# Performance work log

Measured on AMD Instinct MI355X. Metric: run time of the kernel, lower is better.

The kernel has to match this reference:

```python
import jax, jax.numpy as jnp
from jax import lax
import numpy as np

B, N, M, C, K = 2, 16384, 4096, 16, 32
RADIUS = 0.1
EPS = 1e-8


def setup_inputs() -> dict:
    key = jax.random.key(0)
    ks = jax.random.split(key, 9)
    return {
        "xyz": jax.random.uniform(ks[0], (B, N, 3), jnp.float32),
        "new_xyz": jax.random.uniform(ks[1], (B, M, 3), jnp.float32),
        "features": jax.random.normal(ks[2], (B, C, N), jnp.float32),
        "w0": jax.random.normal(ks[3], (32, C), jnp.float32) * 0.1,
        "b0": jax.random.normal(ks[4], (32,), jnp.float32) * 0.1,
        "w1": jax.random.normal(ks[5], (64, 32), jnp.float32) * 0.1,
        "b1": jax.random.normal(ks[6], (64,), jnp.float32) * 0.1,
        "wxyz": jax.random.normal(ks[7], (32, 3), jnp.float32) * 0.1,
        "bxyz": jax.random.normal(ks[8], (32,), jnp.float32) * 0.1,
    }


def ball_query(xyz, new_xyz, radius, nsample):
    """Return (idx [B,M,K] int32, idn multiplicity [B,M,K] int32, has_any [B,M] bool).
    Matches pointnet2 ball_query: first `nsample` in-radius indices (ascending),
    empty slots padded with the first found index; idn counts how many times an
    index is duplicated in a row (0 everywhere for rows with no neighbor)."""
    d2 = jnp.sum((new_xyz[:, :, None, :] - xyz[:, None, :, :]) ** 2, axis=-1)  # B,M,N
    n = xyz.shape[1]
    score = jnp.where(d2 < radius * radius,
                      jnp.arange(n, dtype=jnp.int32), jnp.int32(n))
    idx = -lax.top_k(-score, nsample)[0]          # B,M,K smallest indices, asc
    valid = idx < n
    idx = jnp.where(valid, idx, idx[..., :1])      # pad with first found index
    has_any = valid[..., 0]
    idx = jnp.where(idx >= n, 0, idx)              # safe gather for empty rows
    cnt = jnp.sum(idx[..., :, None] == idx[..., None, :], axis=-1).astype(jnp.int32)
    idn = jnp.where(has_any[..., None], cnt, 0)
    return idx, idn, has_any


def reference(xyz, new_xyz, features, w0, b0, w1, b1, wxyz, bxyz):
    idx, idn, has_any = ball_query(xyz, new_xyz, RADIUS, K)
    b_idx = jnp.arange(xyz.shape[0])[:, None, None]
    # QueryAndGroup: relative coords + gathered features
    rel = xyz[b_idx, idx] - new_xyz[:, :, None, :]            # B,M,K,3
    rel = jnp.transpose(rel, (0, 3, 1, 2))                    # B,3,M,K
    gfeat = jnp.transpose(features, (0, 2, 1))[b_idx, idx]    # B,M,K,C
    gfeat = jnp.transpose(gfeat, (0, 3, 1, 2))                # B,C,M,K

    # distance-reciprocal weights, duplicate-corrected by idn, row-normalized
    dist = jnp.linalg.norm(rel, axis=1, keepdims=True)        # B,1,M,K
    dist_recip = 1.0 / (dist + EPS)
    _idn = jnp.where(has_any[:, None, :, None], idn[:, None, :, :], 1).astype(dist.dtype)
    dist_recip = dist_recip / _idn
    weights = dist_recip / jnp.sum(dist_recip, axis=3, keepdims=True)
    idn_mask = has_any[:, None, :, None].astype(dist.dtype)
    weights = weights * idn_mask                              # zero empty rows

    # SharedMLP on features: 1x1 conv == per-point matmul, ReLU
    h = jax.nn.relu(jnp.einsum('bcmk,oc->bomk', gfeat, w0) + b0[None, :, None, None])
    h = jax.nn.relu(jnp.einsum('bcmk,oc->bomk', h, w1) + b1[None, :, None, None])
    feat_sum = jnp.sum(weights * h, axis=3)                   # B,64,M weighted sum-pool

    # xyz branch: SharedMLP [3,32] + max-pool over neighbors
    hx = jax.nn.relu(jnp.einsum('bcmk,oc->bomk', rel, wxyz) + bxyz[None, :, None, None])
    feat_max = jnp.max(hx, axis=3)                            # B,32,M

    return new_xyz, jnp.concatenate([feat_max, feat_sum], axis=1)  # (B,M,3),(B,96,M)
```

## Files before the change

kernel.cpp:

```cpp
#include <hip/hip_runtime.h>
#include <math.h>
#include <limits.h>

#define BB 2
#define NN 16384
#define MM 4096
#define CCH 16
#define KK 32
#define R2 0.01f
#define EPSV 1e-8f
#define GD 10
#define CPB (GD*GD*GD)
#define CAP 56
#define NCELL (BB*CPB)
#define WSA_OFF 8192
#define WSB_OFF 10240
#define BUCKET_OFF 16384
#define FEATT_OFF (2*1024*1024)
#define WS_GRID (BUCKET_OFF + (size_t)NCELL*CAP*16)
#define WS_FT   (FEATT_OFF + (size_t)BB*NN*CCH*2)
#define NDW 512
#define TBL 768
#define HST 40

typedef __attribute__((ext_vector_type(8))) short short8;
typedef __attribute__((ext_vector_type(4))) float v4f;

__device__ __forceinline__ short f2bf(float f) {
    unsigned u = __float_as_uint(f);
    unsigned r = u + 0x7FFFu + ((u >> 16) & 1u);
    return (short)(r >> 16);
}
__device__ __forceinline__ unsigned pk2(float a, float b) {
    return (unsigned)(unsigned short)f2bf(a) | ((unsigned)(unsigned short)f2bf(b) << 16);
}

__device__ __forceinline__ int cell_of(float x, float y, float z) {
    int cx = min(GD-1, max(0, (int)(x * 10.0f)));
    int cy = min(GD-1, max(0, (int)(y * 10.0f)));
    int cz = min(GD-1, max(0, (int)(z * 10.0f)));
    return (cx*GD + cy)*GD + cz;
}

__global__ void k_scatter(const float* __restrict__ xyz, const float* __restrict__ feat,
                          const float* __restrict__ w0, const float* __restrict__ w1,
                          int* __restrict__ cnt, int* __restrict__ ovf,
                          float4* __restrict__ buckets,
                          short8* __restrict__ wsA, short8* __restrict__ wsB,
                          uint4* __restrict__ ftb, int use_ft) {
    if (blockIdx.x == 0) {
        int t = threadIdx.x;
        if (t < 128) {
            int fi = t >> 6, l = t & 63, l15 = l & 15, qd = (l >> 4) & 3;
            short8 a = {0,0,0,0,0,0,0,0};
            if (qd < 2)
                #pragma unroll
                for (int j = 0; j < 8; ++j)
                    a[j] = f2bf(w0[(fi*16 + l15)*CCH + qd*8 + j]);
            wsA[fi*64 + l] = a;
        }
        if (t < 64) {
            int l15 = t & 15, qd = t >> 4;
            #pragma unroll
            for (int u = 0; u < 4; ++u) {
                const float* wr = w1 + ((u << 4) + l15)*32 + (qd << 3);
                short8 bb;
                #pragma unroll
                for (int j = 0; j < 8; ++j) bb[j] = f2bf(wr[j]);
                wsB[t*4 + u] = bb;
            }
        }
    }
    int i = blockIdx.x*256 + threadIdx.x;
    if (i >= BB*NN) return;
    const float* p = xyz + (size_t)i*3;
    int b = i >> 14;
    int n = i & (NN-1);
    float x = p[0], y = p[1], z = p[2];
    int cell = b*CPB + cell_of(x, y, z);
    int slot = atomicAdd(&cnt[cell], 1);
    if (slot < CAP)
        buckets[(size_t)cell*CAP + slot] = make_float4(x, y, z, __int_as_float(n));
    else
        *ovf = 1;
    if (use_ft) {
        const float* fb = feat + (size_t)b*CCH*NN + n;
        unsigned d[8];
        #pragma unroll
        for (int c2 = 0; c2 < 8; ++c2)
            d[c2] = pk2(fb[(2*c2)*NN], fb[(2*c2+1)*NN]);
        ftb[(size_t)i*2 + 0] = make_uint4(d[0], d[1], d[2], d[3]);
        ftb[(size_t)i*2 + 1] = make_uint4(d[4], d[5], d[6], d[7]);
    }
}

__global__ __launch_bounds__(256, 4) void grouper_fused(
    const float* __restrict__ xyz, const float* __restrict__ new_xyz,
    const float* __restrict__ feat,
    const float* __restrict__ w0, const float* __restrict__ b0,
    const float* __restrict__ w1, const float* __restrict__ b1,
    const float* __restrict__ wxyz, const float* __restrict__ bxyz,
    const int* __restrict__ cnt, const int* __restrict__ ovf,
    const float4* __restrict__ buckets,
    const short8* __restrict__ wsA, const short8* __restrict__ wsB,
    const short8* __restrict__ ftb,
    int use_grid, int use_ft,
    float* __restrict__ out)
{
    const int lane = threadIdx.x & 63;
    const int wid  = threadIdx.x >> 6;
    const int q    = (blockIdx.x << 2) + wid;
    const int b    = q >> 12;
    const int m    = q & (MM - 1);

    __shared__ int s_idx[4][KK];
    __shared__ float4 s_rel[4][KK];
    __shared__ __align__(16) unsigned s_bm[4][NDW];
    __shared__ __align__(16) int s_tbl[4][TBL];

    const float* xb = xyz + (size_t)b * NN * 3;
    const float qx = new_xyz[((size_t)b*MM + m)*3 + 0];
    const float qy = new_xyz[((size_t)b*MM + m)*3 + 1];
    const float qz = new_xyz[((size_t)b*MM + m)*3 + 2];
    const unsigned long long below = (1ull << lane) - 1ull;

    int nfound = 0, idx0 = 0;
    bool need_full = (use_grid == 0) || (use_grid && ovf[0] != 0);

    if (!need_full) {
        uint4 z4 = make_uint4(0u, 0u, 0u, 0u);
        *(uint4*)&s_bm[wid][lane*8]     = z4;
        *(uint4*)&s_bm[wid][lane*8 + 4] = z4;

        int x0 = max(0, (int)floorf((qx - 0.1f)*10.0f - 1e-3f));
        int x1 = min(GD-1, (int)floorf((qx + 0.1f)*10.0f + 1e-3f));
        int y0 = max(0, (int)floorf((qy - 0.1f)*10.0f - 1e-3f));
        int y1 = min(GD-1, (int)floorf((qy + 0.1f)*10.0f + 1e-3f));
        int z0 = max(0, (int)floorf((qz - 0.1f)*10.0f - 1e-3f));
        int z1 = min(GD-1, (int)floorf((qz + 0.1f)*10.0f + 1e-3f));

        const int nzc = z1 - z0 + 1, nyc = y1 - y0 + 1, nxc = x1 - x0 + 1;
        const int nyz = nyc * nzc;
        const int ncells = nxc * nyz;
        int myCnt = 0, myBase = 0;
        if (lane < ncells) {
            const float rnyz = 1.0f / (float)nyz;
            const float rnz  = 1.0f / (float)nzc;
            int cxr = (int)((float)lane * rnyz + 1e-4f);
            int rem = lane - cxr * nyz;
            int cyr = (int)((float)rem * rnz + 1e-4f);
            int czr = rem - cyr * nzc;
            int cx = x0 + cxr, cy = y0 + cyr, cz = z0 + czr;
            float xlo = cx*0.1f, ylo = cy*0.1f, zlo = cz*0.1f;
            float ddx = fmaxf(fmaxf(xlo - qx, qx - (xlo + 0.1f)), 0.0f);
            float ddy = fmaxf(fmaxf(ylo - qy, qy - (ylo + 0.1f)), 0.0f);
            float ddz = fmaxf(fmaxf(zlo - qz, qz - (zlo + 0.1f)), 0.0f);
            if (ddx*ddx + ddy*ddy + ddz*ddz < R2) {
                int cell = b*CPB + (cx*GD + cy)*GD + cz;
                myCnt = min(cnt[cell], CAP);
                myBase = cell*CAP;
            }
        }

        int incl = myCnt;
        #pragma unroll
        for (int d = 1; d < 64; d <<= 1) {
            int t = __shfl_up(incl, d);
            if (lane >= d) incl += t;
        }
        const int total = __shfl(incl, 63);
        const int wbase = incl - myCnt;

        if (total > TBL) {
            need_full = true;
        } else {
            int* tbl = &s_tbl[wid][0];
            for (int t = 0; t < myCnt; ++t) tbl[wbase + t] = myBase + t;
            __builtin_amdgcn_wave_barrier();

            const int iters = (total + 63) >> 6;
            int j = lane;
            bool v0 = (j < total);
            int sl0 = v0 ? tbl[j] : 0;
            float4 p0 = make_float4(0.f, 0.f, 0.f, 0.f);
            if (v0) p0 = buckets[sl0];
            for (int it = 0; it < iters; ++it) {
                int jn = j + 64;
                bool v1 = (jn < total);
                int sl1 = v1 ? tbl[jn] : 0;
                float4 pn = make_float4(0.f, 0.f, 0.f, 0.f);
                if (v1) pn = buckets[sl1];
                if (v0) {
                    float dx = p0.x - qx, dy = p0.y - qy, dz = p0.z - qz;
                    if (dx*dx + dy*dy + dz*dz < R2) {
                        int id = __float_as_int(p0.w);
                        atomicOr(&s_bm[wid][id >> 5], 1u << (id & 31));
                    }
                }
                j = jn; v0 = v1; sl0 = sl1; p0 = pn;
            }

            __builtin_amdgcn_wave_barrier();

            uint4 d0 = *(uint4*)&s_bm[wid][lane*8];
            uint4 d1 = *(uint4*)&s_bm[wid][lane*8 + 4];
            unsigned dw[8] = {d0.x, d0.y, d0.z, d0.w, d1.x, d1.y, d1.z, d1.w};
            int pc = 0;
            #pragma unroll
            for (int jj = 0; jj < 8; ++jj) pc += __popc(dw[jj]);
            int pre = pc;
            #pragma unroll
            for (int d = 1; d < 64; d <<= 1) {
                int t = __shfl_up(pre, d);
                if (lane >= d) pre += t;
            }
            int tt = __shfl(pre, 63);
            int rank = pre - pc;
            nfound = min(tt, KK);

            if (rank < KK) {
                #pragma unroll
                for (int jj = 0; jj < 8; ++jj) {
                    unsigned bits = dw[jj];
                    while (bits && rank < KK) {
                        int bpos = __builtin_ctz(bits);
                        s_idx[wid][rank] = ((lane*8 + jj) << 5) + bpos;
                        bits &= bits - 1;
                        ++rank;
                    }
                }
            }

            __builtin_amdgcn_wave_barrier();
            idx0 = (nfound > 0) ? s_idx[wid][0] : 0;
            __builtin_amdgcn_wave_barrier();
            if (lane >= nfound && lane < KK) s_idx[wid][lane] = idx0;
            __builtin_amdgcn_wave_barrier();
        }
    }

    if (need_full) {
        int cntf = 0;
        for (int basep = 0; basep < NN; basep += 256) {
            float d2a[4];
            #pragma unroll
            for (int j = 0; j < 4; ++j) {
                int i = basep + (j << 6) + lane;
                float px = xb[i*3+0], py = xb[i*3+1], pz = xb[i*3+2];
                float dx = px - qx, dy = py - qy, dz = pz - qz;
                d2a[j] = dx*dx + dy*dy + dz*dz;
            }
            #pragma unroll
            for (int j = 0; j < 4; ++j) {
                bool hit = d2a[j] < R2;
                unsigned long long msk = __ballot(hit);
                if (hit) {
                    int pos = cntf + __popcll(msk & below);
                    if (pos < KK) s_idx[wid][pos] = basep + (j << 6) + lane;
                }
                cntf += __popcll(msk);
            }
            if (cntf >= KK) break;
        }
        nfound = cntf < KK ? cntf : KK;
        __builtin_amdgcn_wave_barrier();
        if (lane < KK) {
            int v = 0;
            if (nfound > 0) v = (lane < nfound) ? s_idx[wid][lane] : s_idx[wid][0];
            s_idx[wid][lane] = v;
        }
        __builtin_amdgcn_wave_barrier();
        idx0 = s_idx[wid][0];
    }

    {
        const int k = lane & 31;
        const int h = lane >> 5;
        const int ik = s_idx[wid][k];
        float px = xb[ik*3+0], py = xb[ik*3+1], pz = xb[ik*3+2];
        float rx = px - qx, ry = py - qy, rz = pz - qz;
        float dist = sqrtf(rx*rx + ry*ry + rz*rz);
        float recip = 1.0f / (dist + EPSV);
        float mult = (float)(1 + KK - nfound);
        float w = recip / ((ik == idx0) ? mult : 1.0f);
        float S = w;
        #pragma unroll
        for (int d = 1; d < 32; d <<= 1) S += __shfl_xor(S, d);
        float wk = (nfound > 0) ? (w / S) : 0.0f;
        if (h == 0) s_rel[wid][k] = make_float4(rx, ry, rz, wk);
    }
    __builtin_amdgcn_wave_barrier();

    const int l15 = lane & 15;
    const int quad = lane >> 4;

    short8 A1, A1b, Bf[4];
    if (use_grid) {
        A1  = wsA[lane];
        A1b = wsA[64 + lane];
        #pragma unroll
        for (int u = 0; u < 4; ++u) Bf[u] = wsB[lane*4 + u];
    } else {
        short8 z = {0,0,0,0,0,0,0,0};
        A1 = z; A1b = z;
        if (quad < 2) {
            #pragma unroll
            for (int j = 0; j < 8; ++j) {
                A1[j]  = f2bf(w0[l15*CCH + quad*8 + j]);
                A1b[j] = f2bf(w0[(16 + l15)*CCH + quad*8 + j]);
            }
        }
        #pragma unroll
        for (int u = 0; u < 4; ++u) {
            const float* wr = w1 + ((u << 4) + l15)*32 + (quad << 3);
            #pragma unroll
            for (int j = 0; j < 8; ++j) Bf[u][j] = f2bf(wr[j]);
        }
    }

    short8 G0 = {0,0,0,0,0,0,0,0}, G1 = {0,0,0,0,0,0,0,0};
    if (quad < 2) {
        int ika = s_idx[wid][l15];
        int ikb = s_idx[wid][16 + l15];
        if (use_ft) {
            G0 = ftb[(size_t)(b*NN + ika)*2 + quad];
            G1 = ftb[(size_t)(b*NN + ikb)*2 + quad];
        } else {
            const float* fb = feat + (size_t)b * CCH * NN;
            int cb0 = quad << 3;
            #pragma unroll
            for (int j = 0; j < 8; ++j) {
                G0[j] = f2bf(fb[(cb0 + j)*NN + ika]);
                G1[j] = f2bf(fb[(cb0 + j)*NN + ikb]);
            }
        }
    }

    v4f C0, C1;
    #pragma unroll
    for (int r = 0; r < 4; ++r) {
        C0[r] = b0[(quad << 2) + r];
        C1[r] = b0[16 + (quad << 2) + r];
    }

    v4f H00 = __builtin_amdgcn_mfma_f32_16x16x32_bf16(A1,  G0, C0, 0, 0, 0);
    v4f H01 = __builtin_amdgcn_mfma_f32_16x16x32_bf16(A1b, G0, C1, 0, 0, 0);
    v4f H10 = __builtin_amdgcn_mfma_f32_16x16x32_bf16(A1,  G1, C0, 0, 0, 0);
    v4f H11 = __builtin_amdgcn_mfma_f32_16x16x32_bf16(A1b, G1, C1, 0, 0, 0);

    __builtin_amdgcn_wave_barrier();
    short* hb = (short*)&s_tbl[wid][0];
    {
        uint2 w;
        w.x = pk2(fmaxf(H00[0],0.f), fmaxf(H00[1],0.f));
        w.y = pk2(fmaxf(H00[2],0.f), fmaxf(H00[3],0.f));
        *(uint2*)&hb[l15*HST + (quad << 2)] = w;
        w.x = pk2(fmaxf(H01[0],0.f), fmaxf(H01[1],0.f));
        w.y = pk2(fmaxf(H01[2],0.f), fmaxf(H01[3],0.f));
        *(uint2*)&hb[l15*HST + 16 + (quad << 2)] = w;
        w.x = pk2(fmaxf(H10[0],0.f), fmaxf(H10[1],0.f));
        w.y = pk2(fmaxf(H10[2],0.f), fmaxf(H10[3],0.f));
        *(uint2*)&hb[(16 + l15)*HST + (quad << 2)] = w;
        w.x = pk2(fmaxf(H11[0],0.f), fmaxf(H11[1],0.f));
        w.y = pk2(fmaxf(H11[2],0.f), fmaxf(H11[3],0.f));
        *(uint2*)&hb[(16 + l15)*HST + 16 + (quad << 2)] = w;
    }
    __builtin_amdgcn_wave_barrier();

    short8 A2_0 = *(short8*)&hb[l15*HST + (quad << 3)];
    short8 A2_1 = *(short8*)&hb[(16 + l15)*HST + (quad << 3)];

    float wkv[2][4];
    #pragma unroll
    for (int t = 0; t < 2; ++t)
        #pragma unroll
        for (int r = 0; r < 4; ++r)
            wkv[t][r] = s_rel[wid][16*t + (quad << 2) + r].w;

    float* out2 = out + (size_t)BB*MM*3 + (size_t)b*96*MM;

    float Su[4];
    #pragma unroll
    for (int u = 0; u < 4; ++u) {
        float b1u = b1[(u << 4) + l15];
        v4f Cb = {b1u, b1u, b1u, b1u};
        v4f D0 = __builtin_amdgcn_mfma_f32_16x16x32_bf16(A2_0, Bf[u], Cb, 0, 0, 0);
        v4f D1 = __builtin_amdgcn_mfma_f32_16x16x32_bf16(A2_1, Bf[u], Cb, 0, 0, 0);
        float s = 0.f;
        #pragma unroll
        for (int r = 0; r < 4; ++r)
            s += wkv[0][r]*fmaxf(D0[r], 0.f) + wkv[1][r]*fmaxf(D1[r], 0.f);
        s += __shfl_xor(s, 16);
        s += __shfl_xor(s, 32);
        Su[u] = s;
    }
    float sout = (quad == 0) ? Su[0] : (quad == 1) ? Su[1] : (quad == 2) ? Su[2] : Su[3];
    out2[(32 + lane)*MM + m] = sout;

    {
        const int c = lane & 31;
        const int h = lane >> 5;
        const float wx0 = wxyz[c*3+0], wx1 = wxyz[c*3+1], wx2 = wxyz[c*3+2];
        const float bc = bxyz[c];
        float v = 0.0f;
        #pragma unroll
        for (int kk = 0; kk < 16; ++kk) {
            float4 hr = s_rel[wid][(h << 4) + kk];
            float t = bc + wx0*hr.x + wx1*hr.y + wx2*hr.z;
            v = fmaxf(v, fmaxf(t, 0.0f));
        }
        v = fmaxf(v, __shfl_xor(v, 32));
        if (h == 0) out2[c*MM + m] = v;
    }

    if (lane == 0) {
        float* o0 = out + ((size_t)b*MM + m)*3;
        o0[0] = qx; o0[1] = qy; o0[2] = qz;
    }
}

extern "C" void kernel_launch(void* const* d_in, const int* in_sizes, int n_in,
                              void* d_out, int out_size, void* d_ws, size_t ws_size,
                              hipStream_t stream) {
    const float* xyz     = (const float*)d_in[0];
    const float* new_xyz = (const float*)d_in[1];
    const float* feat    = (const float*)d_in[2];
    const float* w0      = (const float*)d_in[3];
    const float* b0      = (const float*)d_in[4];
    const float* w1      = (const float*)d_in[5];
    const float* b1      = (const float*)d_in[6];
    const float* wxyz    = (const float*)d_in[7];
    const float* bxyz    = (const float*)d_in[8];
    float* out = (float*)d_out;

    int* ovf = (int*)d_ws;
    int* cnt = (int*)((char*)d_ws + 64);
    short8* wsA = (short8*)((char*)d_ws + WSA_OFF);
    short8* wsB = (short8*)((char*)d_ws + WSB_OFF);
    float4* buckets = (float4*)((char*)d_ws + BUCKET_OFF);
    uint4* ftb4 = (uint4*)((char*)d_ws + FEATT_OFF);
    const short8* ftb = (const short8*)((char*)d_ws + FEATT_OFF);
    const int use_grid = (d_ws != nullptr && ws_size >= WS_GRID) ? 1 : 0;
    const int use_ft   = (d_ws != nullptr && ws_size >= WS_FT) ? 1 : 0;

    if (use_grid) {
        hipMemsetAsync(d_ws, 0, BUCKET_OFF, stream);
        hipLaunchKernelGGL(k_scatter, dim3((BB*NN+255)/256), dim3(256), 0, stream,
                           xyz, feat, w0, w1, cnt, ovf, buckets, wsA, wsB, ftb4, use_ft);
    }
    hipLaunchKernelGGL(grouper_fused, dim3((BB*MM)/4), dim3(256), 0, stream,
                       xyz, new_xyz, feat, w0, b0, w1, b1, wxyz, bxyz,
                       cnt, ovf, buckets, wsA, wsB, ftb, use_grid, use_ft, out);
}
```

Baseline: 96.46 us.

## Share bitmap and table LDS scratch, raise occupancy, deepen bucket prefetch

Merges the per-wave bitmap and cell-slot table into one shared scratch region, shrinking the table cap from 768 to 512 entries, and raises launch bounds from 4 to 8 blocks per CU. The aim is more resident waves to hide the latency of the global bucket gathers. The candidate loop now prefetches two iterations ahead instead of one, and the memset is cut to only the counter/flag region. Queries whose candidate count exceeds 512 now fall back to the slow full scan more often, and the tighter register budget may cause spills.

```diff
diff --git a/kernel.cpp b/kernel.cpp
--- a/kernel.cpp
+++ b/kernel.cpp
@@ -20,7 +20,7 @@
 #define WS_GRID (BUCKET_OFF + (size_t)NCELL*CAP*16)
 #define WS_FT   (FEATT_OFF + (size_t)BB*NN*CCH*2)
 #define NDW 512
-#define TBL 768
+#define TBL 512
 #define HST 40
 
 typedef __attribute__((ext_vector_type(8))) short short8;
@@ -94,7 +94,7 @@
     }
 }
 
-__global__ __launch_bounds__(256, 4) void grouper_fused(
+__global__ __launch_bounds__(256, 8) void grouper_fused(
     const float* __restrict__ xyz, const float* __restrict__ new_xyz,
     const float* __restrict__ feat,
     const float* __restrict__ w0, const float* __restrict__ b0,
@@ -115,8 +115,10 @@
 
     __shared__ int s_idx[4][KK];
     __shared__ float4 s_rel[4][KK];
-    __shared__ __align__(16) unsigned s_bm[4][NDW];
-    __shared__ __align__(16) int s_tbl[4][TBL];
+    __shared__ __align__(16) unsigned s_scr[4][1024];
+
+    unsigned* bm = &s_scr[wid][0];
+    int* tbl = (int*)&s_scr[wid][NDW];
 
     const float* xb = xyz + (size_t)b * NN * 3;
     const float qx = new_xyz[((size_t)b*MM + m)*3 + 0];
@@ -129,8 +131,8 @@
 
     if (!need_full) {
         uint4 z4 = make_uint4(0u, 0u, 0u, 0u);
-        *(uint4*)&s_bm[wid][lane*8]     = z4;
-        *(uint4*)&s_bm[wid][lane*8 + 4] = z4;
+        *(uint4*)&bm[lane*8]     = z4;
+        *(uint4*)&bm[lane*8 + 4] = z4;
 
         int x0 = max(0, (int)floorf((qx - 0.1f)*10.0f - 1e-3f));
         int x1 = min(GD-1, (int)floorf((qx + 0.1f)*10.0f + 1e-3f));
@@ -174,36 +176,41 @@
         if (total > TBL) {
             need_full = true;
         } else {
-            int* tbl = &s_tbl[wid][0];
             for (int t = 0; t < myCnt; ++t) tbl[wbase + t] = myBase + t;
             __builtin_amdgcn_wave_barrier();
 
             const int iters = (total + 63) >> 6;
-            int j = lane;
-            bool v0 = (j < total);
-            int sl0 = v0 ? tbl[j] : 0;
+            int j0 = lane;
+            bool v0 = (j0 < total);
+            int sl0 = v0 ? tbl[j0] : 0;
             float4 p0 = make_float4(0.f, 0.f, 0.f, 0.f);
             if (v0) p0 = buckets[sl0];
+            bool v1 = (j0 + 64 < total);
+            int sl1 = v1 ? tbl[j0 + 64] : 0;
+            float4 p1 = make_float4(0.f, 0.f, 0.f, 0.f);
+            if (v1) p1 = buckets[sl1];
             for (int it = 0; it < iters; ++it) {
-                int jn = j + 64;
-                bool v1 = (jn < total);
-                int sl1 = v1 ? tbl[jn] : 0;
-                float4 pn = make_float4(0.f, 0.f, 0.f, 0.f);
-                if (v1) pn = buckets[sl1];
+                int j2 = j0 + 128;
+                bool v2 = (j2 < total);
+                int sl2 = v2 ? tbl[j2] : 0;
+                float4 p2 = make_float4(0.f, 0.f, 0.f, 0.f);
+                if (v2) p2 = buckets[sl2];
                 if (v0) {
                     float dx = p0.x - qx, dy = p0.y - qy, dz = p0.z - qz;
                     if (dx*dx + dy*dy + dz*dz < R2) {
                         int id = __float_as_int(p0.w);
-                        atomicOr(&s_bm[wid][id >> 5], 1u << (id & 31));
+                        atomicOr(&bm[id >> 5], 1u << (id & 31));
                     }
                 }
-                j = jn; v0 = v1; sl0 = sl1; p0 = pn;
+                j0 += 64;
+                v0 = v1; p0 = p1;
+                v1 = v2; p1 = p2;
             }
 
             __builtin_amdgcn_wave_barrier();
 
-            uint4 d0 = *(uint4*)&s_bm[wid][lane*8];
-            uint4 d1 = *(uint4*)&s_bm[wid][lane*8 + 4];
+            uint4 d0 = *(uint4*)&bm[lane*8];
+            uint4 d1 = *(uint4*)&bm[lane*8 + 4];
             unsigned dw[8] = {d0.x, d0.y, d0.z, d0.w, d1.x, d1.y, d1.z, d1.w};
             int pc = 0;
             #pragma unroll
@@ -349,7 +356,7 @@
     v4f H11 = __builtin_amdgcn_mfma_f32_16x16x32_bf16(A1b, G1, C1, 0, 0, 0);
 
     __builtin_amdgcn_wave_barrier();
-    short* hb = (short*)&s_tbl[wid][0];
+    short* hb = (short*)&s_scr[wid][0];
     {
         uint2 w;
         w.x = pk2(fmaxf(H00[0],0.f), fmaxf(H00[1],0.f));
@@ -444,7 +451,7 @@
     const int use_ft   = (d_ws != nullptr && ws_size >= WS_FT) ? 1 : 0;
 
     if (use_grid) {
-        hipMemsetAsync(d_ws, 0, BUCKET_OFF, stream);
+        hipMemsetAsync(d_ws, 0, 8192, stream);
         hipLaunchKernelGGL(k_scatter, dim3((BB*NN+255)/256), dim3(256), 0, stream,
                            xyz, feat, w0, w1, cnt, ovf, buckets, wsA, wsB, ftb4, use_ft);
     }
```

After: 106.1 us. 10.0% more time.
